# Kernel optimization log

Measured on AMD Instinct MI355X. Metric: run time of the kernel, lower is better.

The kernel has to match this reference:

```python
import jax, jax.numpy as jnp
import numpy as np

B, S, D = 16, 2048, 128

def setup_inputs() -> dict:
    key = jax.random.key(0)
    k1, k2, k3 = jax.random.split(key, 3)
    return {
        "query": jax.random.normal(k1, (B, S, D), dtype=jnp.float32),
        "key": jax.random.normal(k2, (B, S, D), dtype=jnp.float32),
        "value": jax.random.normal(k3, (B, S, D), dtype=jnp.float32),
    }

def reference(query, key, value):
    dq = query.shape[-1]
    dk = key.shape[-1]
    # custom scale: sqrt(Dq) + sqrt(Dk - Dq); with Dq == Dk this is sqrt(Dq)
    inv_scale = np.sqrt(dq) + np.sqrt(dk - dq)
    qk = jnp.einsum("bqd,bkd->bqk", query, key) / jnp.float32(inv_scale)
    attn = jax.nn.softmax(qk, axis=-1)  # dropout_p=0 -> identity
    return jnp.einsum("bqk,bkd->bqd", attn, value)
```

## Files before the change

### kernel.cpp

```cpp
#include <hip/hip_runtime.h>
#include <stdint.h>

#define Bn 16
#define Sn 2048
#define Dn 128
#define QBLK 128
#define KVBLK 64
#define NTHR 512
#define NT (Sn / KVBLK)

typedef __attribute__((ext_vector_type(4))) float f32x4;
typedef __attribute__((ext_vector_type(16))) float f32x16;
typedef __attribute__((ext_vector_type(8))) short bf16x8;
typedef __attribute__((ext_vector_type(2))) unsigned int u32x2;

#define SMEM_BYTES 67584

__device__ __forceinline__ uint32_t f2bf_u(float f) {
  return (__float_as_uint(f) + 0x8000u) >> 16;
}
__device__ __forceinline__ uint32_t pk2(float a, float b) {
  return f2bf_u(a) | (f2bf_u(b) << 16);
}

__global__ __launch_bounds__(256) void tr_kv(const float* __restrict__ K,
                                             const float* __restrict__ V,
                                             unsigned short* __restrict__ Kf,
                                             unsigned short* __restrict__ Vf) {
  __shared__ unsigned short lds[64 * 136];
  const int tid = threadIdx.x;
  const size_t tileoff = (size_t)blockIdx.x * (64 * Dn);

  {
    const float* src = K + tileoff;
#pragma unroll
    for (int it = 0; it < 8; ++it) {
      const int gr = it * 256 + tid;
      const int k = gr >> 5, g4 = gr & 31;
      const float4 v = ((const float4*)src)[gr];
      unsigned short* p = &lds[k * 136 + g4 * 4];
      p[0] = (unsigned short)f2bf_u(v.x);
      p[1] = (unsigned short)f2bf_u(v.y);
      p[2] = (unsigned short)f2bf_u(v.z);
      p[3] = (unsigned short)f2bf_u(v.w);
    }
    __syncthreads();
    char* dst = (char*)Kf + (size_t)blockIdx.x * 16384;
#pragma unroll
    for (int it = 0; it < 4; ++it) {
      const int g = it * 256 + tid;
      const int lane = g & 63, dk = (g >> 6) & 7, h = g >> 9;
      const unsigned short* p =
          &lds[(32 * h + (lane & 31)) * 136 + dk * 16 + 8 * (lane >> 5)];
      uint4 o;
      o.x = (uint32_t)p[0] | ((uint32_t)p[1] << 16);
      o.y = (uint32_t)p[2] | ((uint32_t)p[3] << 16);
      o.z = (uint32_t)p[4] | ((uint32_t)p[5] << 16);
      o.w = (uint32_t)p[6] | ((uint32_t)p[7] << 16);
      *(uint4*)(dst + g * 16) = o;
    }
  }
  __syncthreads();

  {
    const float* src = V + tileoff;
#pragma unroll
    for (int it = 0; it < 8; ++it) {
      const int gr = it * 256 + tid;
      const int k = gr >> 5, g4 = gr & 31;
      const float4 v = ((const float4*)src)[gr];
      unsigned short* p = &lds[k * 136 + g4 * 4];
      p[0] = (unsigned short)f2bf_u(v.x);
      p[1] = (unsigned short)f2bf_u(v.y);
      p[2] = (unsigned short)f2bf_u(v.z);
      p[3] = (unsigned short)f2bf_u(v.w);
    }
    __syncthreads();
    char* dst = (char*)Vf + (size_t)blockIdx.x * 16384;
#pragma unroll
    for (int it = 0; it < 4; ++it) {
      const int g = it * 256 + tid;
      const int lane = g & 63, f3 = (g >> 6) & 7, h = g >> 9;
      const int d = (f3 >> 1) * 32 + (lane & 31);
      const int k0 = 32 * h + (f3 & 1) * 16 + 8 * (lane >> 5);
      uint4 o;
      o.x = (uint32_t)lds[(k0 + 0) * 136 + d] | ((uint32_t)lds[(k0 + 1) * 136 + d] << 16);
      o.y = (uint32_t)lds[(k0 + 2) * 136 + d] | ((uint32_t)lds[(k0 + 3) * 136 + d] << 16);
      o.z = (uint32_t)lds[(k0 + 4) * 136 + d] | ((uint32_t)lds[(k0 + 5) * 136 + d] << 16);
      o.w = (uint32_t)lds[(k0 + 6) * 136 + d] | ((uint32_t)lds[(k0 + 7) * 136 + d] << 16);
      *(uint4*)(dst + g * 16) = o;
    }
  }
}

__global__ __launch_bounds__(NTHR, 2) void attn_fwd(
    const float* __restrict__ Q, const unsigned short* __restrict__ Kf,
    const unsigned short* __restrict__ Vf, float* __restrict__ O) {
  __shared__ uint4 smem_[SMEM_BYTES / 16];
  char* smem = (char*)smem_;

  const int tid = threadIdx.x;
  const int lane = tid & 63;
  const int w = tid >> 6;
  const int qw = w & 3;
  const int h = w >> 2;
  const int hi = lane >> 5;
  const int ql = lane & 31;

  const int i = blockIdx.x;
  const int j = i >> 3;
  const int b = (i & 7) + 8 * (j & 1);
  const int q0 = (j >> 1) * QBLK;
  const int qg = q0 + qw * 32 + ql;

  const float qscale = 0.08838834764831845f * 1.44269504088896340736f;
  bf16x8 qf[8];
  {
    const float* qrow = Q + (size_t)(b * Sn + qg) * Dn;
#pragma unroll
    for (int dk = 0; dk < 8; ++dk) {
      const int d0 = dk * 16 + hi * 8;
      const float4 a = *(const float4*)(qrow + d0);
      const float4 d = *(const float4*)(qrow + d0 + 4);
      bf16x8 q8;
      q8[0] = (short)f2bf_u(a.x * qscale); q8[1] = (short)f2bf_u(a.y * qscale);
      q8[2] = (short)f2bf_u(a.z * qscale); q8[3] = (short)f2bf_u(a.w * qscale);
      q8[4] = (short)f2bf_u(d.x * qscale); q8[5] = (short)f2bf_u(d.y * qscale);
      q8[6] = (short)f2bf_u(d.z * qscale); q8[7] = (short)f2bf_u(d.w * qscale);
      qf[dk] = q8;
    }
  }

  f32x16 o[4];
#pragma unroll
  for (int dt = 0; dt < 4; ++dt) {
#pragma unroll
    for (int jj = 0; jj < 16; ++jj) o[dt][jj] = 0.f;
  }
  float l_r = 0.f;

  const char* Kg = (const char*)(Kf + (size_t)b * Sn * Dn);
  const char* Vg = (const char*)(Vf + (size_t)b * Sn * Dn);

#define LOADK(kd_, t_)                                                         \
  {                                                                            \
    const char* kt = Kg + (size_t)(t_)*16384 + h * 8192 + lane * 16;           \
    _Pragma("unroll") for (int f = 0; f < 8; ++f)                              \
        kd_[f] = *(const bf16x8*)(kt + f * 1024);                              \
  }

#define TILE(kf_, t_)                                                          \
  {                                                                            \
    bf16x8 vfr[8];                                                             \
    {                                                                          \
      const char* vt = Vg + (size_t)(t_)*16384 + h * 8192 + lane * 16;         \
      _Pragma("unroll") for (int f = 0; f < 8; ++f)                            \
          vfr[f] = *(const bf16x8*)(vt + f * 1024);                            \
    }                                                                          \
    f32x16 s;                                                                  \
    _Pragma("unroll") for (int jj = 0; jj < 16; ++jj) s[jj] = -8.0f;           \
    __builtin_amdgcn_s_setprio(1);                                             \
    _Pragma("unroll") for (int dk = 0; dk < 8; ++dk)                           \
        s = __builtin_amdgcn_mfma_f32_32x32x16_bf16(kf_[dk], qf[dk], s, 0, 0, 0);\
    __builtin_amdgcn_s_setprio(0);                                             \
    _Pragma("unroll") for (int jj = 0; jj < 16; ++jj)                          \
        s[jj] = __builtin_amdgcn_exp2f(s[jj]);                                 \
    {                                                                          \
      float r0 = 0.f, r1 = 0.f, r2 = 0.f, r3 = 0.f;                            \
      _Pragma("unroll") for (int jj = 0; jj < 4; ++jj) {                       \
        r0 += s[jj]; r1 += s[4 + jj]; r2 += s[8 + jj]; r3 += s[12 + jj];       \
      }                                                                        \
      l_r += (r0 + r1) + (r2 + r3);      \
    }                                                                          \
    uint32_t own[4][2];                                                        \
    _Pragma("unroll") for (int mm = 0; mm < 4; ++mm) {                         \
      own[mm][0] = pk2(s[4 * mm + 0], s[4 * mm + 1]);                          \
      own[mm][1] = pk2(s[4 * mm + 2], s[4 * mm + 3]);                          \
    }                                                                          \
    uint32_t rcv[2][2];                                                        \
    _Pragma("unroll") for (int jj = 0; jj < 2; ++jj)                           \
        _Pragma("unroll") for (int e = 0; e < 2; ++e) {                        \
      uint32_t sel = hi ? own[2 * jj][e] : own[2 * jj + 1][e];                 \
      rcv[jj][e] = (uint32_t)__shfl_xor((int)sel, 32, 64);                     \
    }                                                                          \
    bf16x8 pb[2];                                                              \
    _Pragma("unroll") for (int ks = 0; ks < 2; ++ks) {                         \
      union { uint32_t u[4]; bf16x8 v; } tt;                                   \
      tt.u[0] = hi ? rcv[ks][0] : own[2 * ks][0];                              \
      tt.u[1] = hi ? rcv[ks][1] : own[2 * ks][1];                              \
      tt.u[2] = hi ? own[2 * ks + 1][0] : rcv[ks][0];                          \
      tt.u[3] = hi ? own[2 * ks + 1][1] : rcv[ks][1];                          \
      pb[ks] = tt.v;                                                           \
    }                                                                          \
    __builtin_amdgcn_s_setprio(1);                                             \
    _Pragma("unroll") for (int dt = 0; dt < 4; ++dt) {                         \
      _Pragma("unroll") for (int ks = 0; ks < 2; ++ks) {                       \
        o[dt] = __builtin_amdgcn_mfma_f32_32x32x16_bf16(vfr[dt * 2 + ks],      \
                                                        pb[ks], o[dt], 0, 0, 0);\
      }                                                                        \
    }                                                                          \
    __builtin_amdgcn_s_setprio(0);                                             \
  }

  bf16x8 kC[8], kN[8];
  LOADK(kC, 0)
  __builtin_amdgcn_sched_barrier(0);
  for (int t = 0; t < NT; t += 2) {
    LOADK(kN, t + 1)
    __builtin_amdgcn_sched_barrier(0);
    TILE(kC, t)
    if (t + 2 < NT) {
      LOADK(kC, t + 2)
    }
    __builtin_amdgcn_sched_barrier(0);
    TILE(kN, t + 1)
  }

  l_r += __shfl_xor(l_r, 32, 64);
  __syncthreads();
  char* xch = smem + qw * 16896;
  if (h) {
#pragma unroll
    for (int dt = 0; dt < 4; ++dt) {
#pragma unroll
      for (int q2 = 0; q2 < 4; ++q2) {
        float4 v;
        v.x = o[dt][4 * q2 + 0]; v.y = o[dt][4 * q2 + 1];
        v.z = o[dt][4 * q2 + 2]; v.w = o[dt][4 * q2 + 3];
        *(float4*)(xch + (dt * 4 + q2) * 1024 + lane * 16) = v;
      }
    }
    *(float*)(xch + 16384 + lane * 4) = l_r;
  }
  __syncthreads();
  if (!h) {
    const float l1 = *(const float*)(xch + 16384 + lane * 4);
    const float inv = 1.0f / (l_r + l1);
    float* orow = O + (size_t)(b * Sn + qg) * Dn;
#pragma unroll
    for (int dt = 0; dt < 4; ++dt) {
#pragma unroll
      for (int q2 = 0; q2 < 4; ++q2) {
        const float4 o1v =
            *(const float4*)(xch + (dt * 4 + q2) * 1024 + lane * 16);
        float4 v;
        v.x = (o[dt][4 * q2 + 0] + o1v.x) * inv;
        v.y = (o[dt][4 * q2 + 1] + o1v.y) * inv;
        v.z = (o[dt][4 * q2 + 2] + o1v.z) * inv;
        v.w = (o[dt][4 * q2 + 3] + o1v.w) * inv;
        *(float4*)(orow + dt * 32 + q2 * 8 + hi * 4) = v;
      }
    }
  }
}

extern "C" void kernel_launch(void* const* d_in, const int* in_sizes, int n_in,
                              void* d_out, int out_size, void* d_ws, size_t ws_size,
                              hipStream_t stream) {
  (void)in_sizes; (void)n_in; (void)out_size; (void)ws_size;
  const float* Q = (const float*)d_in[0];
  const float* K = (const float*)d_in[1];
  const float* V = (const float*)d_in[2];
  float* O = (float*)d_out;

  const size_t nE = (size_t)Bn * Sn * Dn;
  unsigned short* Kf = (unsigned short*)d_ws;
  unsigned short* Vf = Kf + nE;

  tr_kv<<<dim3(Bn * 32, 1, 1), dim3(256, 1, 1), 0, stream>>>(K, V, Kf, Vf);
  attn_fwd<<<dim3((Sn / QBLK) * Bn, 1, 1), dim3(NTHR, 1, 1), 0, stream>>>(
      Q, Kf, Vf, O);
}
```

Measured before the change: 61.29 us.

## Process two KV tiles jointly with interleaved QK MFMAs and deeper K/V prefetch

Restructures the main loop so each iteration handles two KV tiles together. The QK^T MFMA chains for both tiles are interleaved, which hides MFMA dependency latency. Both K tiles for the next pair are prefetched while V for the current pair is loaded. The softmax/pack stage and the PV MFMAs are then batched for both tiles. This adds register pressure (two K and two V fragment sets plus two score accumulators), which may reduce occupancy.

Result: slower. 111.8 us (+82.4%).

```diff
diff --git a/kernel.cpp b/kernel.cpp
--- a/kernel.cpp
+++ b/kernel.cpp
@@ -148,34 +148,28 @@
     _Pragma("unroll") for (int f = 0; f < 8; ++f)                              \
         kd_[f] = *(const bf16x8*)(kt + f * 1024);                              \
   }
-
-#define TILE(kf_, t_)                                                          \
+#define LOADV(vd_, t_)                                                         \
   {                                                                            \
-    bf16x8 vfr[8];                                                             \
-    {                                                                          \
-      const char* vt = Vg + (size_t)(t_)*16384 + h * 8192 + lane * 16;         \
-      _Pragma("unroll") for (int f = 0; f < 8; ++f)                            \
-          vfr[f] = *(const bf16x8*)(vt + f * 1024);                            \
-    }                                                                          \
-    f32x16 s;                                                                  \
-    _Pragma("unroll") for (int jj = 0; jj < 16; ++jj) s[jj] = -8.0f;           \
-    __builtin_amdgcn_s_setprio(1);                                             \
-    _Pragma("unroll") for (int dk = 0; dk < 8; ++dk)                           \
-        s = __builtin_amdgcn_mfma_f32_32x32x16_bf16(kf_[dk], qf[dk], s, 0, 0, 0);\
-    __builtin_amdgcn_s_setprio(0);                                             \
+    const char* vt = Vg + (size_t)(t_)*16384 + h * 8192 + lane * 16;           \
+    _Pragma("unroll") for (int f = 0; f < 8; ++f)                              \
+        vd_[f] = *(const bf16x8*)(vt + f * 1024);                              \
+  }
+
+#define SMPACK(s_, pb_)                                                        \
+  {                                                                            \
     _Pragma("unroll") for (int jj = 0; jj < 16; ++jj)                          \
-        s[jj] = __builtin_amdgcn_exp2f(s[jj]);                                 \
+        s_[jj] = __builtin_amdgcn_exp2f(s_[jj]);                               \
     {                                                                          \
       float r0 = 0.f, r1 = 0.f, r2 = 0.f, r3 = 0.f;                            \
       _Pragma("unroll") for (int jj = 0; jj < 4; ++jj) {                       \
-        r0 += s[jj]; r1 += s[4 + jj]; r2 += s[8 + jj]; r3 += s[12 + jj];       \
+        r0 += s_[jj]; r1 += s_[4 + jj]; r2 += s_[8 + jj]; r3 += s_[12 + jj];   \
       }                                                                        \
-      l_r += (r0 + r1) + (r2 + r3);      \
+      l_r += (r0 + r1) + (r2 + r3);                                            \
     }                                                                          \
     uint32_t own[4][2];                                                        \
     _Pragma("unroll") for (int mm = 0; mm < 4; ++mm) {                         \
-      own[mm][0] = pk2(s[4 * mm + 0], s[4 * mm + 1]);                          \
-      own[mm][1] = pk2(s[4 * mm + 2], s[4 * mm + 3]);                          \
+      own[mm][0] = pk2(s_[4 * mm + 0], s_[4 * mm + 1]);                        \
+      own[mm][1] = pk2(s_[4 * mm + 2], s_[4 * mm + 3]);                        \
     }                                                                          \
     uint32_t rcv[2][2];                                                        \
     _Pragma("unroll") for (int jj = 0; jj < 2; ++jj)                           \
@@ -183,37 +177,59 @@
       uint32_t sel = hi ? own[2 * jj][e] : own[2 * jj + 1][e];                 \
       rcv[jj][e] = (uint32_t)__shfl_xor((int)sel, 32, 64);                     \
     }                                                                          \
-    bf16x8 pb[2];                                                              \
     _Pragma("unroll") for (int ks = 0; ks < 2; ++ks) {                         \
       union { uint32_t u[4]; bf16x8 v; } tt;                                   \
       tt.u[0] = hi ? rcv[ks][0] : own[2 * ks][0];                              \
       tt.u[1] = hi ? rcv[ks][1] : own[2 * ks][1];                              \
       tt.u[2] = hi ? own[2 * ks + 1][0] : rcv[ks][0];                          \
       tt.u[3] = hi ? own[2 * ks + 1][1] : rcv[ks][1];                          \
-      pb[ks] = tt.v;                                                           \
-    }                                                                          \
-    __builtin_amdgcn_s_setprio(1);                                             \
-    _Pragma("unroll") for (int dt = 0; dt < 4; ++dt) {                         \
-      _Pragma("unroll") for (int ks = 0; ks < 2; ++ks) {                       \
-        o[dt] = __builtin_amdgcn_mfma_f32_32x32x16_bf16(vfr[dt * 2 + ks],      \
-                                                        pb[ks], o[dt], 0, 0, 0);\
-      }                                                                        \
-    }                                                                          \
-    __builtin_amdgcn_s_setprio(0);                                             \
-  }
-
-  bf16x8 kC[8], kN[8];
-  LOADK(kC, 0)
+      pb_[ks] = tt.v;                                                          \
+    }                                                                          \
+  }
+
+  bf16x8 kA[8], kB[8], vA[8], vB[8];
+  LOADK(kA, 0)
+  LOADK(kB, 1)
   __builtin_amdgcn_sched_barrier(0);
   for (int t = 0; t < NT; t += 2) {
-    LOADK(kN, t + 1)
+    LOADV(vA, t)
     __builtin_amdgcn_sched_barrier(0);
-    TILE(kC, t)
+
+    f32x16 sA, sB;
+#pragma unroll
+    for (int jj = 0; jj < 16; ++jj) { sA[jj] = -8.0f; sB[jj] = -8.0f; }
+    __builtin_amdgcn_s_setprio(1);
+#pragma unroll
+    for (int dk = 0; dk < 8; ++dk) {
+      sA = __builtin_amdgcn_mfma_f32_32x32x16_bf16(kA[dk], qf[dk], sA, 0, 0, 0);
+      sB = __builtin_amdgcn_mfma_f32_32x32x16_bf16(kB[dk], qf[dk], sB, 0, 0, 0);
+    }
+    __builtin_amdgcn_s_setprio(0);
+
     if (t + 2 < NT) {
-      LOADK(kC, t + 2)
-    }
+      LOADK(kA, t + 2)
+      LOADK(kB, t + 3)
+    }
+    LOADV(vB, t + 1)
     __builtin_amdgcn_sched_barrier(0);
-    TILE(kN, t + 1)
+
+    bf16x8 pbA[2], pbB[2];
+    SMPACK(sA, pbA)
+    SMPACK(sB, pbB)
+
+    __builtin_amdgcn_s_setprio(1);
+#pragma unroll
+    for (int dt = 0; dt < 4; ++dt) {
+#pragma unroll
+      for (int ks = 0; ks < 2; ++ks)
+        o[dt] = __builtin_amdgcn_mfma_f32_32x32x16_bf16(vA[dt * 2 + ks], pbA[ks],
+                                                        o[dt], 0, 0, 0);
+#pragma unroll
+      for (int ks = 0; ks < 2; ++ks)
+        o[dt] = __builtin_amdgcn_mfma_f32_32x32x16_bf16(vB[dt * 2 + ks], pbB[ks],
+                                                        o[dt], 0, 0, 0);
+    }
+    __builtin_amdgcn_s_setprio(0);
   }
 
   l_r += __shfl_xor(l_r, 32, 64);
```

## Stage K/V tiles through double-buffered LDS with async global_load_lds

Applied to the files above, without the earlier changes.

Each K/V tile is now loaded cooperatively by all waves into double-buffered LDS using global_load_lds, and the MFMA operands are read from LDS. Previously each wave loaded its K and V fragments straight from global memory into registers. The change is meant to cut redundant global traffic across waves that share a batch, to overlap the next tile's load with compute, and to free K-prefetch registers. In exchange it adds a block-wide __syncthreads per tile and extra LDS reads. It also drops the two-tile register-level software pipelining.

Result: faster. 58.71 us (-4.2%).

```diff
diff --git a/kernel.cpp b/kernel.cpp
--- a/kernel.cpp
+++ b/kernel.cpp
@@ -14,6 +14,7 @@
 typedef __attribute__((ext_vector_type(8))) short bf16x8;
 typedef __attribute__((ext_vector_type(2))) unsigned int u32x2;
 
+#define BUFSZ 32768
 #define SMEM_BYTES 67584
 
 __device__ __forceinline__ uint32_t f2bf_u(float f) {
@@ -142,27 +143,43 @@
   const char* Kg = (const char*)(Kf + (size_t)b * Sn * Dn);
   const char* Vg = (const char*)(Vf + (size_t)b * Sn * Dn);
 
-#define LOADK(kd_, t_)                                                         \
+#define STAGE(dst_, t_)                                                        \
   {                                                                            \
-    const char* kt = Kg + (size_t)(t_)*16384 + h * 8192 + lane * 16;           \
-    _Pragma("unroll") for (int f = 0; f < 8; ++f)                              \
-        kd_[f] = *(const bf16x8*)(kt + f * 1024);                              \
-  }
-
-#define TILE(kf_, t_)                                                          \
+    const char* gk = Kg + (size_t)(t_)*16384 + w * 2048 + lane * 16;           \
+    const char* gv = Vg + (size_t)(t_)*16384 + w * 2048 + lane * 16;           \
+    char* lk = smem + (dst_) + w * 2048;                                       \
+    char* lv = smem + (dst_) + 16384 + w * 2048;                               \
+    _Pragma("unroll") for (int it = 0; it < 2; ++it) {                         \
+      __builtin_amdgcn_global_load_lds(                                        \
+          (const __attribute__((address_space(1))) uint32_t*)(gk + it * 1024), \
+          (__attribute__((address_space(3))) uint32_t*)(lk + it * 1024),       \
+          16, 0, 0);                                                           \
+      __builtin_amdgcn_global_load_lds(                                        \
+          (const __attribute__((address_space(1))) uint32_t*)(gv + it * 1024), \
+          (__attribute__((address_space(3))) uint32_t*)(lv + it * 1024),       \
+          16, 0, 0);                                                           \
+    }                                                                          \
+  }
+
+#define TILE(cb_)                                                              \
   {                                                                            \
     bf16x8 vfr[8];                                                             \
     {                                                                          \
-      const char* vt = Vg + (size_t)(t_)*16384 + h * 8192 + lane * 16;         \
+      const char* vt = smem + (cb_) + 16384 + h * 8192 + lane * 16;            \
       _Pragma("unroll") for (int f = 0; f < 8; ++f)                            \
           vfr[f] = *(const bf16x8*)(vt + f * 1024);                            \
     }                                                                          \
     f32x16 s;                                                                  \
     _Pragma("unroll") for (int jj = 0; jj < 16; ++jj) s[jj] = -8.0f;           \
-    __builtin_amdgcn_s_setprio(1);                                             \
-    _Pragma("unroll") for (int dk = 0; dk < 8; ++dk)                           \
-        s = __builtin_amdgcn_mfma_f32_32x32x16_bf16(kf_[dk], qf[dk], s, 0, 0, 0);\
-    __builtin_amdgcn_s_setprio(0);                                             \
+    {                                                                          \
+      const char* kt = smem + (cb_) + h * 8192 + lane * 16;                    \
+      __builtin_amdgcn_s_setprio(1);                                           \
+      _Pragma("unroll") for (int dk = 0; dk < 8; ++dk) {                       \
+        bf16x8 kfr = *(const bf16x8*)(kt + dk * 1024);                         \
+        s = __builtin_amdgcn_mfma_f32_32x32x16_bf16(kfr, qf[dk], s, 0, 0, 0);  \
+      }                                                                        \
+      __builtin_amdgcn_s_setprio(0);                                           \
+    }                                                                          \
     _Pragma("unroll") for (int jj = 0; jj < 16; ++jj)                          \
         s[jj] = __builtin_amdgcn_exp2f(s[jj]);                                 \
     {                                                                          \
@@ -202,22 +219,17 @@
     __builtin_amdgcn_s_setprio(0);                                             \
   }
 
-  bf16x8 kC[8], kN[8];
-  LOADK(kC, 0)
-  __builtin_amdgcn_sched_barrier(0);
-  for (int t = 0; t < NT; t += 2) {
-    LOADK(kN, t + 1)
+  STAGE(0, 0)
+  __syncthreads();
+  for (int t = 0; t < NT; ++t) {
+    const uint32_t cb = (uint32_t)(t & 1) * BUFSZ;
+    if (t + 1 < NT) STAGE(BUFSZ - cb, t + 1)
     __builtin_amdgcn_sched_barrier(0);
-    TILE(kC, t)
-    if (t + 2 < NT) {
-      LOADK(kC, t + 2)
-    }
-    __builtin_amdgcn_sched_barrier(0);
-    TILE(kN, t + 1)
+    TILE(cb)
+    __syncthreads();
   }
 
   l_r += __shfl_xor(l_r, 32, 64);
-  __syncthreads();
   char* xch = smem + qw * 16896;
   if (h) {
 #pragma unroll
```
